# Performance work log

Hardware: AMD Instinct MI355X
Metric: run time of the kernel (lower is better)

## Reference

```python
import jax, jax.numpy as jnp
import numpy as np

B, L, D = 2, 512, 1024
INNER = 32
PAIR = 128


def setup_inputs() -> dict:
    key = jax.random.key(0)
    ks = jax.random.split(key, 6)
    scale = lambda fan_in: 1.0 / np.sqrt(fan_in)
    return {
        "sequence_state": jax.random.normal(ks[0], (B, L, D), dtype=jnp.float32),
        "ln_gamma": jnp.ones((D,), dtype=jnp.float32),
        "ln_beta": jnp.zeros((D,), dtype=jnp.float32),
        "W_proj": jax.random.normal(ks[1], (2 * INNER, D), dtype=jnp.float32) * scale(D),
        "b_proj": jnp.zeros((2 * INNER,), dtype=jnp.float32),
        "W_o": jax.random.normal(ks[2], (PAIR, 2 * INNER), dtype=jnp.float32) * scale(2 * INNER),
        "b_o": jnp.zeros((PAIR,), dtype=jnp.float32),
    }


def reference(sequence_state, ln_gamma, ln_beta, W_proj, b_proj, W_o, b_o):
    eps = 1e-5
    # LayerNorm over last dim
    mu = jnp.mean(sequence_state, axis=-1, keepdims=True)
    var = jnp.mean(jnp.square(sequence_state - mu), axis=-1, keepdims=True)
    s = (sequence_state - mu) * jax.lax.rsqrt(var + eps) * ln_gamma + ln_beta
    # proj: B x L x 2*inner
    s = jnp.einsum("bld,ed->ble", s, W_proj) + b_proj
    q, k = jnp.split(s, 2, axis=-1)  # each B x L x inner
    # broadcast outer product / difference: B x L x L x inner
    prod = q[:, None, :, :] * k[:, :, None, :]
    diff = q[:, None, :, :] - k[:, :, None, :]
    x = jnp.concatenate([prod, diff], axis=-1)  # B x L x L x 2*inner
    # o_proj: B x L x L x pairwise
    x = jnp.einsum("bije,pe->bijp", x, W_o) + b_o
    return x
```

## Files before the change

### kernel.cpp

```cpp
#include <hip/hip_runtime.h>
#include <hip/hip_bf16.h>
#include <stdint.h>


typedef __attribute__((ext_vector_type(8))) short short8;
typedef __attribute__((ext_vector_type(4))) float floatx4;

__device__ __forceinline__ unsigned short f2bf(float f) {
    union { float f; unsigned int u; } v; v.f = f;
    return (unsigned short)((v.u + 0x7FFFu + ((v.u >> 16) & 1u)) >> 16);
}

__device__ __forceinline__ floatx4 fmadd4(float s, floatx4 w, floatx4 a) {
    a.x += s * w.x; a.y += s * w.y; a.z += s * w.z; a.w += s * w.w; return a;
}

__global__ __launch_bounds__(256) void k0_transpose(
    const float* __restrict__ Wproj, const float* __restrict__ Wo,
    float* __restrict__ Wt, float* __restrict__ Wot, float* __restrict__ Wdt)
{
    int g = blockIdx.x * 256 + threadIdx.x;
    if (g < 65536) {
        int o = g >> 10, d = g & 1023;
        Wt[d * 64 + o] = Wproj[g];
    } else {
        int h = g - 65536;
        int p = h & 127, e = h >> 7;
        float v = Wo[p * 64 + e];
        if (e < 32) Wot[e * 128 + p] = v;
        else        Wdt[(e - 32) * 128 + p] = v;
    }
}

__global__ __launch_bounds__(256) void k1_ln_proj(
    const float* __restrict__ x, const float* __restrict__ gamma, const float* __restrict__ beta,
    const float* __restrict__ Wt, const float* __restrict__ b_proj,
    const float* __restrict__ Wdt, const float* __restrict__ b_o,
    unsigned short* __restrict__ Qbf, float* __restrict__ Kf, float* __restrict__ C0)
{
    __shared__ __attribute__((aligned(16))) float s_sh[4][1024];
    __shared__ __attribute__((aligned(16))) float part[4][16][68];
    __shared__ float k_sh[4][32];

    const int t = threadIdx.x;
    const int w = t >> 6;
    const int lane = t & 63;
    const int row = blockIdx.x * 4 + w;

    const float* xr = x + (size_t)row * 1024;
    floatx4 xv[4];
    float sum = 0.f, sq = 0.f;
#pragma unroll
    for (int c = 0; c < 4; ++c) {
        xv[c] = *(const floatx4*)(xr + (c * 64 + lane) * 4);
        sum += xv[c].x + xv[c].y + xv[c].z + xv[c].w;
        sq  += xv[c].x * xv[c].x + xv[c].y * xv[c].y + xv[c].z * xv[c].z + xv[c].w * xv[c].w;
    }
#pragma unroll
    for (int m = 1; m < 64; m <<= 1) {
        sum += __shfl_xor(sum, m, 64);
        sq  += __shfl_xor(sq,  m, 64);
    }
    const float mu   = sum * (1.f / 1024.f);
    const float var  = sq * (1.f / 1024.f) - mu * mu;
    const float rsig = rsqrtf(var + 1e-5f);
#pragma unroll
    for (int c = 0; c < 4; ++c) {
        int d = (c * 64 + lane) * 4;
        floatx4 g4 = *(const floatx4*)(gamma + d);
        floatx4 b4 = *(const floatx4*)(beta + d);
        floatx4 s4;
        s4.x = (xv[c].x - mu) * rsig * g4.x + b4.x;
        s4.y = (xv[c].y - mu) * rsig * g4.y + b4.y;
        s4.z = (xv[c].z - mu) * rsig * g4.z + b4.z;
        s4.w = (xv[c].w - mu) * rsig * g4.w + b4.w;
        *(floatx4*)(&s_sh[w][d]) = s4;
    }
    __syncthreads();

    {
        const int o4 = t & 15;
        const int ch = t >> 4;
        const floatx4* Wt4 = (const floatx4*)Wt;
        floatx4 a0 = {0.f, 0.f, 0.f, 0.f}, a1 = a0, a2 = a0, a3 = a0;
        const int dbase = ch * 64;
#pragma unroll 8
        for (int dd = 0; dd < 64; ++dd) {
            const int d = dbase + dd;
            floatx4 w4 = Wt4[d * 16 + o4];
            a0 = fmadd4(s_sh[0][d], w4, a0);
            a1 = fmadd4(s_sh[1][d], w4, a1);
            a2 = fmadd4(s_sh[2][d], w4, a2);
            a3 = fmadd4(s_sh[3][d], w4, a3);
        }
        *(floatx4*)&part[0][ch][o4 * 4] = a0;
        *(floatx4*)&part[1][ch][o4 * 4] = a1;
        *(floatx4*)&part[2][ch][o4 * 4] = a2;
        *(floatx4*)&part[3][ch][o4 * 4] = a3;
    }
    __syncthreads();

    {
        const int r = t >> 6, oo = t & 63;
        float v = b_proj[oo];
#pragma unroll
        for (int c = 0; c < 16; ++c) v += part[r][c][oo];
        const int rowr = blockIdx.x * 4 + r;
        if (oo < 32) {
            Qbf[rowr * 32 + oo] = f2bf(v);
        } else {
            Kf[rowr * 32 + (oo - 32)] = v;
            k_sh[r][oo - 32] = v;
        }
    }
    __syncthreads();

    {
        const int p = t & 127;
        const int r0 = t >> 7;
#pragma unroll
        for (int rr = 0; rr < 2; ++rr) {
            const int r = r0 * 2 + rr;
            float a = 0.f;
#pragma unroll 8
            for (int e = 0; e < 32; ++e) a += k_sh[r][e] * Wdt[e * 128 + p];
            C0[(size_t)(blockIdx.x * 4 + r) * 128 + p] = b_o[p] - a;
        }
    }
}

__global__ __launch_bounds__(256) void k2_pair(
    const unsigned short* __restrict__ Qbf, const float* __restrict__ Kf,
    const float* __restrict__ C0, const float* __restrict__ Wot, const float* __restrict__ Wdt,
    float* __restrict__ out)
{
    __shared__ unsigned short G[32 * 136];
    __shared__ __attribute__((aligned(16))) float T[4][16][132];
    __shared__ float c0s[128];
    __shared__ float ksh[32];

    const int t    = threadIdx.x;
    const int bi   = blockIdx.x >> 1;
    const int half = blockIdx.x & 1;
    const int b    = bi >> 9;

    if (t < 32)  ksh[t] = Kf[(size_t)bi * 32 + t];
    if (t < 128) c0s[t] = C0[(size_t)bi * 128 + t];
    __syncthreads();

#pragma unroll
    for (int it = 0; it < 16; ++it) {
        int idx = it * 256 + t;
        int e = idx >> 7, p = idx & 127;
        float gv = ksh[e] * Wot[idx] + Wdt[idx];
        G[e * 136 + p] = f2bf(gv);
    }
    __syncthreads();

    const int wave = t >> 6, lane = t & 63;
    const int col = lane & 15, quad = lane >> 4;

    short8 bfrag[8];
#pragma unroll
    for (int pt = 0; pt < 8; ++pt) {
        short8 f;
#pragma unroll
        for (int u = 0; u < 8; ++u)
            f[u] = (short)G[(quad * 8 + u) * 136 + pt * 16 + col];
        bfrag[pt] = f;
    }
    float cv[8];
#pragma unroll
    for (int pt = 0; pt < 8; ++pt) cv[pt] = c0s[pt * 16 + col];

    const size_t outbase = (size_t)bi * (512 * 128);
    float (*Tw)[132] = T[wave];

    for (int l = 0; l < 4; ++l) {
        const int jt = half * 16 + wave * 4 + l;
        const int j0 = jt * 16;
        const short8 afrag =
            *(const short8*)(Qbf + ((size_t)b * 512 + j0 + col) * 32 + quad * 8);
        floatx4 acc[8];
#pragma unroll
        for (int pt = 0; pt < 8; ++pt) {
            floatx4 c;
            c.x = cv[pt]; c.y = cv[pt]; c.z = cv[pt]; c.w = cv[pt];
            acc[pt] = __builtin_amdgcn_mfma_f32_16x16x32_bf16(afrag, bfrag[pt], c, 0, 0, 0);
        }
#pragma unroll
        for (int pt = 0; pt < 8; ++pt) {
#pragma unroll
            for (int r = 0; r < 4; ++r)
                Tw[quad * 4 + r][pt * 16 + col] = acc[pt][r];
        }
        float* orow = out + outbase + (size_t)j0 * 128;
#pragma unroll
        for (int s = 0; s < 8; ++s) {
            int idx = s * 64 + lane;
            int rr = idx >> 5, c4 = idx & 31;
            floatx4 v = *(const floatx4*)&Tw[rr][c4 * 4];
            __builtin_nontemporal_store(v, (floatx4*)(orow + rr * 128 + c4 * 4));
        }
    }
}

extern "C" void kernel_launch(void* const* d_in, const int* in_sizes, int n_in,
                              void* d_out, int out_size, void* d_ws, size_t ws_size,
                              hipStream_t stream) {
    const float* x     = (const float*)d_in[0];
    const float* gamma = (const float*)d_in[1];
    const float* beta  = (const float*)d_in[2];
    const float* Wproj = (const float*)d_in[3];
    const float* bproj = (const float*)d_in[4];
    const float* Wo    = (const float*)d_in[5];
    const float* bo    = (const float*)d_in[6];
    float* out = (float*)d_out;

    float* ws = (float*)d_ws;
    float* Wt  = ws;
    float* Wot = ws + 65536;
    float* Wdt = ws + 69632;
    float* Kf  = ws + 73728;
    float* C0  = ws + 106496;
    unsigned short* Qbf = (unsigned short*)(ws + 237568);

    hipLaunchKernelGGL(k0_transpose, dim3(288), dim3(256), 0, stream,
                       Wproj, Wo, Wt, Wot, Wdt);
    hipLaunchKernelGGL(k1_ln_proj, dim3(256), dim3(256), 0, stream,
                       x, gamma, beta, Wt, bproj, Wdt, bo, Qbf, Kf, C0);
    hipLaunchKernelGGL(k2_pair, dim3(2048), dim3(256), 0, stream,
                       Qbf, Kf, C0, Wot, Wdt, out);
}
```

Measured before the change: 284.9 us.

## Swap MFMA operands to store output directly, drop LDS transpose staging

The pair kernel now computes the transposed MFMA product (G as A, Q as B), so each lane holds four consecutive output channels and writes them straight to global memory. This removes the per-tile LDS staging buffer and its extra read/write traffic. Each block now covers all 512 j for one i, halving the block count and building G once per i instead of twice. G is built with vectorized reads of Wo directly, and the Wot transpose is dropped from the prep kernel.

```diff
diff --git a/kernel.cpp b/kernel.cpp
--- a/kernel.cpp
+++ b/kernel.cpp
@@ -17,7 +17,7 @@
 
 __global__ __launch_bounds__(256) void k0_transpose(
     const float* __restrict__ Wproj, const float* __restrict__ Wo,
-    float* __restrict__ Wt, float* __restrict__ Wot, float* __restrict__ Wdt)
+    float* __restrict__ Wt, float* __restrict__ Wdt)
 {
     int g = blockIdx.x * 256 + threadIdx.x;
     if (g < 65536) {
@@ -25,10 +25,8 @@
         Wt[d * 64 + o] = Wproj[g];
     } else {
         int h = g - 65536;
-        int p = h & 127, e = h >> 7;
-        float v = Wo[p * 64 + e];
-        if (e < 32) Wot[e * 128 + p] = v;
-        else        Wdt[(e - 32) * 128 + p] = v;
+        int e = h >> 7, p = h & 127;
+        Wdt[h] = Wo[p * 64 + 32 + e];
     }
 }
 
@@ -129,78 +127,65 @@
     }
 }
 
-__global__ __launch_bounds__(256) void k2_pair(
+__global__ __launch_bounds__(256, 4) void k2_pair(
     const unsigned short* __restrict__ Qbf, const float* __restrict__ Kf,
-    const float* __restrict__ C0, const float* __restrict__ Wot, const float* __restrict__ Wdt,
+    const float* __restrict__ C0, const float* __restrict__ Wo,
     float* __restrict__ out)
 {
-    __shared__ unsigned short G[32 * 136];
-    __shared__ __attribute__((aligned(16))) float T[4][16][132];
-    __shared__ float c0s[128];
-    __shared__ float ksh[32];
-
-    const int t    = threadIdx.x;
-    const int bi   = blockIdx.x >> 1;
-    const int half = blockIdx.x & 1;
-    const int b    = bi >> 9;
-
-    if (t < 32)  ksh[t] = Kf[(size_t)bi * 32 + t];
-    if (t < 128) c0s[t] = C0[(size_t)bi * 128 + t];
-    __syncthreads();
-
-#pragma unroll
-    for (int it = 0; it < 16; ++it) {
-        int idx = it * 256 + t;
-        int e = idx >> 7, p = idx & 127;
-        float gv = ksh[e] * Wot[idx] + Wdt[idx];
-        G[e * 136 + p] = f2bf(gv);
+    __shared__ __attribute__((aligned(16))) unsigned short G2[128 * 40];
+
+    const int t  = threadIdx.x;
+    const int bi = blockIdx.x;
+    const int b  = bi >> 9;
+
+    {
+        const int p  = t >> 1;
+        const int eh = (t & 1) * 16;
+        const float* kp = Kf + (size_t)bi * 32 + eh;
+        const float* wp = Wo + p * 64 + eh;
+        unsigned short g[16];
+#pragma unroll
+        for (int c = 0; c < 4; ++c) {
+            floatx4 kc  = *(const floatx4*)(kp + c * 4);
+            floatx4 wpc = *(const floatx4*)(wp + c * 4);
+            floatx4 wdc = *(const floatx4*)(wp + 32 + c * 4);
+            g[c * 4 + 0] = f2bf(kc.x * wpc.x + wdc.x);
+            g[c * 4 + 1] = f2bf(kc.y * wpc.y + wdc.y);
+            g[c * 4 + 2] = f2bf(kc.z * wpc.z + wdc.z);
+            g[c * 4 + 3] = f2bf(kc.w * wpc.w + wdc.w);
+        }
+        short8 lo, hi;
+#pragma unroll
+        for (int u = 0; u < 8; ++u) { lo[u] = (short)g[u]; hi[u] = (short)g[8 + u]; }
+        *(short8*)(&G2[p * 40 + eh])     = lo;
+        *(short8*)(&G2[p * 40 + eh + 8]) = hi;
     }
     __syncthreads();
 
     const int wave = t >> 6, lane = t & 63;
     const int col = lane & 15, quad = lane >> 4;
 
-    short8 bfrag[8];
-#pragma unroll
-    for (int pt = 0; pt < 8; ++pt) {
-        short8 f;
-#pragma unroll
-        for (int u = 0; u < 8; ++u)
-            f[u] = (short)G[(quad * 8 + u) * 136 + pt * 16 + col];
-        bfrag[pt] = f;
-    }
-    float cv[8];
-#pragma unroll
-    for (int pt = 0; pt < 8; ++pt) cv[pt] = c0s[pt * 16 + col];
-
-    const size_t outbase = (size_t)bi * (512 * 128);
-    float (*Tw)[132] = T[wave];
-
-    for (int l = 0; l < 4; ++l) {
-        const int jt = half * 16 + wave * 4 + l;
-        const int j0 = jt * 16;
-        const short8 afrag =
-            *(const short8*)(Qbf + ((size_t)b * 512 + j0 + col) * 32 + quad * 8);
-        floatx4 acc[8];
+    short8 gfrag[8];
+#pragma unroll
+    for (int pt = 0; pt < 8; ++pt)
+        gfrag[pt] = *(const short8*)(&G2[(pt * 16 + col) * 40 + quad * 8]);
+
+    floatx4 cv[8];
+#pragma unroll
+    for (int pt = 0; pt < 8; ++pt)
+        cv[pt] = *(const floatx4*)(C0 + (size_t)bi * 128 + pt * 16 + quad * 4);
+
+    float* outb = out + (size_t)bi * (512 * 128) + (size_t)col * 128 + quad * 4;
+    const unsigned short* qb = Qbf + ((size_t)b * 512 + col) * 32 + quad * 8;
+
+    for (int l = 0; l < 8; ++l) {
+        const int j0 = (wave * 8 + l) * 16;
+        const short8 afrag = *(const short8*)(qb + (size_t)j0 * 32);
+        float* orow = outb + (size_t)j0 * 128;
 #pragma unroll
         for (int pt = 0; pt < 8; ++pt) {
-            floatx4 c;
-            c.x = cv[pt]; c.y = cv[pt]; c.z = cv[pt]; c.w = cv[pt];
-            acc[pt] = __builtin_amdgcn_mfma_f32_16x16x32_bf16(afrag, bfrag[pt], c, 0, 0, 0);
-        }
-#pragma unroll
-        for (int pt = 0; pt < 8; ++pt) {
-#pragma unroll
-            for (int r = 0; r < 4; ++r)
-                Tw[quad * 4 + r][pt * 16 + col] = acc[pt][r];
-        }
-        float* orow = out + outbase + (size_t)j0 * 128;
-#pragma unroll
-        for (int s = 0; s < 8; ++s) {
-            int idx = s * 64 + lane;
-            int rr = idx >> 5, c4 = idx & 31;
-            floatx4 v = *(const floatx4*)&Tw[rr][c4 * 4];
-            __builtin_nontemporal_store(v, (floatx4*)(orow + rr * 128 + c4 * 4));
+            floatx4 acc = __builtin_amdgcn_mfma_f32_16x16x32_bf16(gfrag[pt], afrag, cv[pt], 0, 0, 0);
+            __builtin_nontemporal_store(acc, (floatx4*)(orow + pt * 16));
         }
     }
 }
@@ -219,16 +204,15 @@
 
     float* ws = (float*)d_ws;
     float* Wt  = ws;
-    float* Wot = ws + 65536;
-    float* Wdt = ws + 69632;
-    float* Kf  = ws + 73728;
-    float* C0  = ws + 106496;
-    unsigned short* Qbf = (unsigned short*)(ws + 237568);
-
-    hipLaunchKernelGGL(k0_transpose, dim3(288), dim3(256), 0, stream,
-                       Wproj, Wo, Wt, Wot, Wdt);
+    float* Wdt = ws + 65536;
+    float* Kf  = ws + 69632;
+    float* C0  = ws + 102400;
+    unsigned short* Qbf = (unsigned short*)(ws + 233472);
+
+    hipLaunchKernelGGL(k0_transpose, dim3(272), dim3(256), 0, stream,
+                       Wproj, Wo, Wt, Wdt);
     hipLaunchKernelGGL(k1_ln_proj, dim3(256), dim3(256), 0, stream,
                        x, gamma, beta, Wt, bproj, Wdt, bo, Qbf, Kf, C0);
-    hipLaunchKernelGGL(k2_pair, dim3(2048), dim3(256), 0, stream,
-                       Qbf, Kf, C0, Wot, Wdt, out);
-}
+    hipLaunchKernelGGL(k2_pair, dim3(1024), dim3(256), 0, stream,
+                       Qbf, Kf, C0, Wo, out);
+}
```

Measured after the change: 326.5 us. 1.15x slower.
